# Kernel optimization log

Measured on AMD Instinct MI355X. Metric: run time of the kernel, lower is better.

The kernel has to match this reference:

```python
import jax, jax.numpy as jnp
import numpy as np

N_NODES = 50000
N_EDGES = 800000
IN_CH = 10
HID = 32
HEADS = 4
OUT_CH = 64
EDIM = 1
NEG_SLOPE = 0.2  # PyG GATv2Conv default
LN_EPS = 1e-5


def _glorot(key, shape):
    fan_in, fan_out = shape[0], shape[-1]
    lim = np.sqrt(6.0 / (fan_in + fan_out))
    return jax.random.uniform(key, shape, jnp.float32, -lim, lim)


def setup_inputs() -> dict:
    key = jax.random.key(0)
    ks = jax.random.split(key, 16)
    x = jax.random.normal(ks[0], (N_NODES, IN_CH), jnp.float32)
    edge_index = jax.random.randint(ks[1], (2, N_EDGES), 0, N_NODES, jnp.int64)
    edge_attr = jax.random.normal(ks[2], (N_EDGES, EDIM), jnp.float32)
    return {
        "x": x,
        "edge_attr": edge_attr,
        "W1l": _glorot(ks[3], (IN_CH, HEADS * HID)),
        "W1r": _glorot(ks[4], (IN_CH, HEADS * HID)),
        "W1e": _glorot(ks[5], (EDIM, HEADS * HID)),
        "att1": _glorot(ks[6], (HEADS, HID)),
        "b1": jnp.zeros((HEADS * HID,), jnp.float32),
        "ln1_g": jnp.ones((HEADS * HID,), jnp.float32),
        "ln1_b": jnp.zeros((HEADS * HID,), jnp.float32),
        "W2l": _glorot(ks[7], (HEADS * HID, OUT_CH)),
        "W2r": _glorot(ks[8], (HEADS * HID, OUT_CH)),
        "W2e": _glorot(ks[9], (EDIM, OUT_CH)),
        "att2": _glorot(ks[10], (1, OUT_CH)),
        "b2": jnp.zeros((OUT_CH,), jnp.float32),
        "ln2_g": jnp.ones((OUT_CH,), jnp.float32),
        "ln2_b": jnp.zeros((OUT_CH,), jnp.float32),
        "edge_index": edge_index,
    }


def gatv2_layer(x, src, dst, edge_attr, Wl, Wr, We, att, bias, heads, ch, concat):
    # GATv2: e_ij = att . leaky_relu(Wl x_i + Wr x_j + We e_ij), softmax over j->i
    n = x.shape[0]
    xl = (x @ Wl).reshape(n, heads, ch)          # target projection [N,H,C]
    xr = (x @ Wr).reshape(n, heads, ch)          # source projection [N,H,C]
    ee = (edge_attr @ We).reshape(-1, heads, ch)  # [E,H,C]
    e = jax.nn.leaky_relu(xl[dst] + xr[src] + ee, NEG_SLOPE)  # [E,H,C]
    logit = jnp.einsum('ehc,hc->eh', e, att)     # [E,H]
    m = jax.ops.segment_max(logit, dst, num_segments=n)       # [N,H]
    expv = jnp.exp(logit - m[dst])
    denom = jax.ops.segment_sum(expv, dst, num_segments=n)    # [N,H]
    alpha = expv / denom[dst]                                  # [E,H]
    out = jax.ops.segment_sum(alpha[:, :, None] * xr[src], dst, num_segments=n)  # [N,H,C]
    out = out.reshape(n, heads * ch) if concat else out.mean(axis=1)
    return out + bias


def layer_norm(h, g, b):
    mu = h.mean(axis=-1, keepdims=True)
    var = ((h - mu) ** 2).mean(axis=-1, keepdims=True)
    return (h - mu) * jax.lax.rsqrt(var + LN_EPS) * g + b


def reference(x, edge_attr, W1l, W1r, W1e, att1, b1, ln1_g, ln1_b,
              W2l, W2r, W2e, att2, b2, ln2_g, ln2_b, edge_index):
    src, dst = edge_index[0], edge_index[1]
    h = gatv2_layer(x, src, dst, edge_attr, W1l, W1r, W1e, att1, b1, HEADS, HID, True)
    h = jax.nn.elu(layer_norm(h, ln1_g, ln1_b))
    # dropout is identity in eval mode
    h = gatv2_layer(h, src, dst, edge_attr, W2l, W2r, W2e, att2, b2, 1, OUT_CH, False)
    h = jax.nn.elu(layer_norm(h, ln2_g, ln2_b))
    return h
```

## Files before the change

kernel.cpp:

```cpp
#include <hip/hip_runtime.h>
#include <math.h>

#define NN 50000
#define NE 800000
#define IN_CH 10
#define NEGS 0.2f
#define LNEPS 1e-5f
#define LOG2E 1.4426950408889634f
#define CH_BLOCKS 782
#define NBUK 196

typedef float f2 __attribute__((ext_vector_type(2)));

__device__ __forceinline__ f2 pkfma(f2 a, f2 b, f2 c) {
    return __builtin_elementwise_fma(a, b, c);
}
__device__ __forceinline__ float red16g(float v) {
    v += __shfl_xor(v, 1);  v += __shfl_xor(v, 2);
    v += __shfl_xor(v, 4);  v += __shfl_xor(v, 8);
    return v;
}
__device__ __forceinline__ float red32g(float v) {
    v = red16g(v); v += __shfl_xor(v, 16);
    return v;
}

__device__ __forceinline__ unsigned pack_bf16(float a, float b) {
    unsigned ua = __float_as_uint(a);
    unsigned ub = __float_as_uint(b);
    ua = (ua + 0x7FFFu + ((ua >> 16) & 1u)) >> 16;
    ub = (ub + 0x7FFFu + ((ub >> 16) & 1u)) & 0xFFFF0000u;
    return ua | ub;
}
__device__ __forceinline__ float bf_lo(unsigned d) { return __uint_as_float(d << 16); }
__device__ __forceinline__ float bf_hi(unsigned d) { return __uint_as_float(d & 0xFFFF0000u); }

__global__ __launch_bounds__(256) void k_proj1(
    const float* __restrict__ x, const float* __restrict__ Wl,
    const float* __restrict__ Wr, float* __restrict__ xl, unsigned* __restrict__ xrb) {
    int lane = threadIdx.x & 63;
    int n = blockIdx.x * 4 + (threadIdx.x >> 6);
    if (n >= NN) return;
    int c0 = lane * 2;
    float al0 = 0.f, al1 = 0.f, ar0 = 0.f, ar1 = 0.f;
#pragma unroll
    for (int k = 0; k < IN_CH; ++k) {
        float xv = x[n * IN_CH + k];
        al0 = fmaf(xv, Wl[k * 128 + c0], al0);
        al1 = fmaf(xv, Wl[k * 128 + c0 + 1], al1);
        ar0 = fmaf(xv, Wr[k * 128 + c0], ar0);
        ar1 = fmaf(xv, Wr[k * 128 + c0 + 1], ar1);
    }
    *(float2*)&xl[(size_t)n * 128 + c0] = make_float2(al0, al1);
    xrb[(size_t)n * 64 + lane] = pack_bf16(ar0, ar1);
}


__global__ __launch_bounds__(256) void k_hist(
    const int* __restrict__ ei, int* __restrict__ bh) {
    __shared__ int h[256];
    int t = threadIdx.x, b = blockIdx.x;
    h[t] = 0;
    __syncthreads();
    int e0 = b * 1024 + t * 4;
    if (e0 < NE) {
        int4 d4 = *(const int4*)(ei + NE + e0);
        atomicAdd(&h[d4.x >> 8], 1);
        atomicAdd(&h[d4.y >> 8], 1);
        atomicAdd(&h[d4.z >> 8], 1);
        atomicAdd(&h[d4.w >> 8], 1);
    }
    __syncthreads();
    bh[b * 256 + t] = h[t];
}

__global__ __launch_bounds__(256) void k_colscan(
    int* __restrict__ bh, int* __restrict__ coltotal) {
    __shared__ int sh[256];
    int t = threadIdx.x, j = blockIdx.x;
    int v[4];
    int mysum = 0;
#pragma unroll
    for (int i = 0; i < 4; ++i) {
        int r = t * 4 + i;
        v[i] = (r < CH_BLOCKS) ? bh[r * 256 + j] : 0;
        mysum += v[i];
    }
    sh[t] = mysum;
    __syncthreads();
    for (int off = 1; off < 256; off <<= 1) {
        int u = (t >= off) ? sh[t - off] : 0;
        __syncthreads();
        sh[t] += u;
        __syncthreads();
    }
    int ex = sh[t] - mysum;
#pragma unroll
    for (int i = 0; i < 4; ++i) {
        int r = t * 4 + i;
        if (r < CH_BLOCKS) { bh[r * 256 + j] = ex; ex += v[i]; }
    }
    if (t == 255) coltotal[j] = sh[255];
}

__global__ __launch_bounds__(256) void k_bb(
    const int* __restrict__ coltotal, int* __restrict__ bb) {
    __shared__ int sh[256];
    int t = threadIdx.x;
    int v = coltotal[t];
    sh[t] = v;
    __syncthreads();
    for (int off = 1; off < 256; off <<= 1) {
        int u = (t >= off) ? sh[t - off] : 0;
        __syncthreads();
        sh[t] += u;
        __syncthreads();
    }
    bb[t] = sh[t] - v;
    if (t == 255) bb[256] = sh[255];
}

__global__ __launch_bounds__(256) void k_coarse(
    const int* __restrict__ ei, const float* __restrict__ ea,
    const int* __restrict__ bh, const int* __restrict__ bb,
    int2* __restrict__ coarse) {
    __shared__ int h[256];
    __shared__ int lbase[256];
    int t = threadIdx.x, b = blockIdx.x;
    h[t] = 0;
    lbase[t] = bb[t] + bh[b * 256 + t];
    __syncthreads();
    int e0 = b * 1024 + t * 4;
    if (e0 >= NE) return;
    int4 d4 = *(const int4*)(ei + NE + e0);
    int4 s4 = *(const int4*)(ei + e0);
    float4 a4 = *(const float4*)(ea + e0);
    {
        int bk = d4.x >> 8; int r = atomicAdd(&h[bk], 1);
        coarse[lbase[bk] + r] = make_int2(s4.x | ((d4.x & 255) << 16), __float_as_int(a4.x));
    }
    {
        int bk = d4.y >> 8; int r = atomicAdd(&h[bk], 1);
        coarse[lbase[bk] + r] = make_int2(s4.y | ((d4.y & 255) << 16), __float_as_int(a4.y));
    }
    {
        int bk = d4.z >> 8; int r = atomicAdd(&h[bk], 1);
        coarse[lbase[bk] + r] = make_int2(s4.z | ((d4.z & 255) << 16), __float_as_int(a4.z));
    }
    {
        int bk = d4.w >> 8; int r = atomicAdd(&h[bk], 1);
        coarse[lbase[bk] + r] = make_int2(s4.w | ((d4.w & 255) << 16), __float_as_int(a4.w));
    }
}

__global__ __launch_bounds__(256) void k_fine(
    const int2* __restrict__ coarse, const int* __restrict__ bb,
    int* __restrict__ rowstart, int2* __restrict__ cpack) {
    __shared__ int cnt[256];
    __shared__ int pfx[256];
    __shared__ int sh[256];
    int t = threadIdx.x, b = blockIdx.x;
    cnt[t] = 0;
    __syncthreads();
    int lo = bb[b], hi = bb[b + 1];
    int ecnt = hi - lo;
    for (int i = t; i < ecnt; i += 256) {
        int dl = (coarse[lo + i].x >> 16) & 255;
        atomicAdd(&cnt[dl], 1);
    }
    __syncthreads();
    int v = cnt[t];
    sh[t] = v;
    __syncthreads();
    for (int off = 1; off < 256; off <<= 1) {
        int u = (t >= off) ? sh[t - off] : 0;
        __syncthreads();
        sh[t] += u;
        __syncthreads();
    }
    pfx[t] = sh[t] - v;
    int n0 = b * 256;
    if (n0 + t < NN) rowstart[n0 + t] = lo + (sh[t] - v);
    if (b == 0 && t == 0) rowstart[NN] = NE;
    cnt[t] = 0;
    __syncthreads();
    for (int i = t; i < ecnt; i += 256) {
        int2 c = coarse[lo + i];
        int dl = (c.x >> 16) & 255;
        int r = atomicAdd(&cnt[dl], 1);
        cpack[lo + pfx[dl] + r] = make_int2(c.x & 0xFFFF, c.y);
    }
}

__global__ __launch_bounds__(256) void k_proj2(
    const float* __restrict__ h1, const float* __restrict__ Wl,
    const float* __restrict__ Wr, float* __restrict__ xl2, unsigned* __restrict__ xr2b) {
    __shared__ float sh_h[64][36];
    __shared__ float sh_w[32][128];
    int t = threadIdx.x;
    int cg = t & 15, ng = t >> 4;
    int c0 = cg * 8;
    int nb = blockIdx.x * 64;
    float acc[4][8];
#pragma unroll
    for (int j = 0; j < 4; ++j)
#pragma unroll
        for (int i = 0; i < 8; ++i) acc[j][i] = 0.f;

    for (int kc = 0; kc < 128; kc += 32) {
#pragma unroll
        for (int i = 0; i < 2; ++i) {
            int fi = t + i * 256;
            int nl = fi >> 3, kq = fi & 7;
            int n = nb + nl;
            float4 v = make_float4(0.f, 0.f, 0.f, 0.f);
            if (n < NN) v = *(const float4*)&h1[(size_t)n * 128 + kc + kq * 4];
            *(float4*)&sh_h[nl][kq * 4] = v;
        }
#pragma unroll
        for (int i = 0; i < 4; ++i) {
            int fi = t + i * 256;
            int kl = fi >> 5, col = (fi & 31) * 4;
            const float* src = (col < 64) ? &Wl[(size_t)(kc + kl) * 64 + col]
                                          : &Wr[(size_t)(kc + kl) * 64 + col - 64];
            *(float4*)&sh_w[kl][col] = *(const float4*)src;
        }
        __syncthreads();
#pragma unroll
        for (int kl = 0; kl < 32; kl += 4) {
            float4 hv[4];
#pragma unroll
            for (int j = 0; j < 4; ++j) hv[j] = *(const float4*)&sh_h[ng + j * 16][kl];
#pragma unroll
            for (int kk = 0; kk < 4; ++kk) {
                float4 wa = *(const float4*)&sh_w[kl + kk][c0];
                float4 wb = *(const float4*)&sh_w[kl + kk][c0 + 4];
#pragma unroll
                for (int j = 0; j < 4; ++j) {
                    float hs = kk == 0 ? hv[j].x : kk == 1 ? hv[j].y : kk == 2 ? hv[j].z : hv[j].w;
                    acc[j][0] = fmaf(hs, wa.x, acc[j][0]);
                    acc[j][1] = fmaf(hs, wa.y, acc[j][1]);
                    acc[j][2] = fmaf(hs, wa.z, acc[j][2]);
                    acc[j][3] = fmaf(hs, wa.w, acc[j][3]);
                    acc[j][4] = fmaf(hs, wb.x, acc[j][4]);
                    acc[j][5] = fmaf(hs, wb.y, acc[j][5]);
                    acc[j][6] = fmaf(hs, wb.z, acc[j][6]);
                    acc[j][7] = fmaf(hs, wb.w, acc[j][7]);
                }
            }
        }
        __syncthreads();
    }
    if (cg < 8) {
#pragma unroll
        for (int j = 0; j < 4; ++j) {
            int n = nb + ng + j * 16;
            if (n < NN) {
                *(float4*)&xl2[(size_t)n * 64 + c0] =
                    make_float4(acc[j][0], acc[j][1], acc[j][2], acc[j][3]);
                *(float4*)&xl2[(size_t)n * 64 + c0 + 4] =
                    make_float4(acc[j][4], acc[j][5], acc[j][6], acc[j][7]);
            }
        }
    } else {
        int cc = c0 - 64;
#pragma unroll
        for (int j = 0; j < 4; ++j) {
            int n = nb + ng + j * 16;
            if (n < NN) {
                uint4 pk;
                pk.x = pack_bf16(acc[j][0], acc[j][1]);
                pk.y = pack_bf16(acc[j][2], acc[j][3]);
                pk.z = pack_bf16(acc[j][4], acc[j][5]);
                pk.w = pack_bf16(acc[j][6], acc[j][7]);
                *(uint4*)&xr2b[(size_t)n * 32 + (cc >> 1)] = pk;
            }
        }
    }
}


__device__ __forceinline__ void edge1_step(
    const int2* __restrict__ cpack, const unsigned char* __restrict__ xrb, int p, int l,
    const f2& xl01, const f2& xl23, const f2& We01, const f2& We23,
    const f2& at6a, const f2& at6b, const f2& at4a, const f2& at4b,
    f2& acc01, f2& acc23, float& den, bool tail, int pmax) {
    bool valid = !tail || (p <= pmax);
    int2 pk = cpack[valid ? p : pmax];
    float eav = __int_as_float(pk.y);
    unsigned off = (unsigned)pk.x * 256u + (unsigned)(l * 8);
    uint2 dw = *(const uint2*)(xrb + off);
    f2 x01, x23;
    x01.x = bf_lo(dw.x); x01.y = bf_hi(dw.x);
    x23.x = bf_lo(dw.y); x23.y = bf_hi(dw.y);
    f2 ev = {eav, eav};
    f2 u01 = pkfma(ev, We01, xl01) + x01;
    f2 u23 = pkfma(ev, We23, xl23) + x23;
    float dot = fmaf(at6a.x, u01.x, at4a.x * fabsf(u01.x));
    dot = fmaf(at6a.y, u01.y, fmaf(at4a.y, fabsf(u01.y), dot));
    dot = fmaf(at6b.x, u23.x, fmaf(at4b.x, fabsf(u23.x), dot));
    dot = fmaf(at6b.y, u23.y, fmaf(at4b.y, fabsf(u23.y), dot));
    dot += __shfl_xor(dot, 1);
    dot += __shfl_xor(dot, 2);
    dot += __shfl_xor(dot, 4);
    float el = exp2f(dot);
    if (tail && !valid) el = 0.f;
    den += el;
    f2 el2 = {el, el};
    acc01 = pkfma(el2, x01, acc01);
    acc23 = pkfma(el2, x23, acc23);
}

__global__ __launch_bounds__(256) void k_fused1(
    const int* __restrict__ rs, const int2* __restrict__ cpack,
    const float* __restrict__ xl, const unsigned char* __restrict__ xrb,
    const float* __restrict__ We, const float* __restrict__ att,
    const float* __restrict__ bias, const float* __restrict__ g,
    const float* __restrict__ b, float* __restrict__ h1) {
    int lane = threadIdx.x & 63;
    int n = blockIdx.x * 4 + (threadIdx.x >> 6);
    if (n >= NN) return;
    int half = lane >> 5;
    int l = lane & 31;
    int c0 = l * 4;
    float4 xldf = *(const float4*)&xl[(size_t)n * 128 + c0];
    float4 Wef = *(const float4*)&We[c0];
    float4 atv = *(const float4*)&att[c0];
    f2 xl01 = {xldf.x, xldf.y}, xl23 = {xldf.z, xldf.w};
    f2 We01 = {Wef.x, Wef.y}, We23 = {Wef.z, Wef.w};
    f2 at6a = {atv.x * (0.6f * LOG2E), atv.y * (0.6f * LOG2E)};
    f2 at6b = {atv.z * (0.6f * LOG2E), atv.w * (0.6f * LOG2E)};
    f2 at4a = {atv.x * (0.4f * LOG2E), atv.y * (0.4f * LOG2E)};
    f2 at4b = {atv.z * (0.4f * LOG2E), atv.w * (0.4f * LOG2E)};
    int beg = rs[n], end = rs[n + 1];
    int cnt = end - beg;
    int pfull = beg + (cnt & ~7);
    f2 a01[2] = {{0.f, 0.f}, {0.f, 0.f}};
    f2 a23[2] = {{0.f, 0.f}, {0.f, 0.f}};
    float den[2] = {0.f, 0.f};
    for (int p0 = beg; p0 < pfull; p0 += 8) {
#pragma unroll
        for (int s = 0; s < 4; ++s)
            edge1_step(cpack, xrb, p0 + s * 2 + half, l, xl01, xl23, We01, We23,
                       at6a, at6b, at4a, at4b, a01[s & 1], a23[s & 1], den[s & 1],
                       false, 0);
    }
    if (cnt & 7) {
#pragma unroll
        for (int s = 0; s < 4; ++s)
            edge1_step(cpack, xrb, pfull + s * 2 + half, l, xl01, xl23, We01, We23,
                       at6a, at6b, at4a, at4b, a01[s & 1], a23[s & 1], den[s & 1],
                       true, end - 1);
    }
    f2 s01 = a01[0] + a01[1];
    f2 s23 = a23[0] + a23[1];
    float den0 = den[0] + den[1];
    s01.x += __shfl_xor(s01.x, 32);
    s01.y += __shfl_xor(s01.y, 32);
    s23.x += __shfl_xor(s23.x, 32);
    s23.y += __shfl_xor(s23.y, 32);
    den0 += __shfl_xor(den0, 32);
    float inv = den0 > 0.f ? 1.f / den0 : 0.f;
    float4 bv = *(const float4*)&bias[c0];
    float a0 = s01.x * inv + bv.x;
    float a1 = s01.y * inv + bv.y;
    float a2 = s23.x * inv + bv.z;
    float a3 = s23.y * inv + bv.w;
    float mu = red32g(a0 + a1 + a2 + a3) * (1.f / 128.f);
    float d0 = a0 - mu, d1 = a1 - mu, d2 = a2 - mu, d3 = a3 - mu;
    float var = red32g(d0 * d0 + d1 * d1 + d2 * d2 + d3 * d3) * (1.f / 128.f);
    float rsq = rsqrtf(var + LNEPS);
    float4 gv = *(const float4*)&g[c0];
    float4 bb = *(const float4*)&b[c0];
    float o0 = d0 * rsq * gv.x + bb.x;
    float o1 = d1 * rsq * gv.y + bb.y;
    float o2 = d2 * rsq * gv.z + bb.z;
    float o3 = d3 * rsq * gv.w + bb.w;
    o0 = o0 > 0.f ? o0 : __expf(o0) - 1.f;
    o1 = o1 > 0.f ? o1 : __expf(o1) - 1.f;
    o2 = o2 > 0.f ? o2 : __expf(o2) - 1.f;
    o3 = o3 > 0.f ? o3 : __expf(o3) - 1.f;
    if (half == 0)
        *(float4*)&h1[(size_t)n * 128 + c0] = make_float4(o0, o1, o2, o3);
}

__device__ __forceinline__ void edge2_step(
    const int2* __restrict__ cpack, const unsigned char* __restrict__ xr2b, int p, int l,
    const f2& xl01, const f2& xl23, const f2& We01, const f2& We23,
    const f2& at6a, const f2& at6b, const f2& at4a, const f2& at4b,
    f2& acc01, f2& acc23, float& den, bool tail, int pmax) {
    bool valid = !tail || (p <= pmax);
    int2 pk = cpack[valid ? p : pmax];
    float eav = __int_as_float(pk.y);
    unsigned off = (unsigned)pk.x * 128u + (unsigned)(l * 8);
    uint2 dw = *(const uint2*)(xr2b + off);
    f2 x01, x23;
    x01.x = bf_lo(dw.x); x01.y = bf_hi(dw.x);
    x23.x = bf_lo(dw.y); x23.y = bf_hi(dw.y);
    f2 ev = {eav, eav};
    f2 u01 = pkfma(ev, We01, xl01) + x01;
    f2 u23 = pkfma(ev, We23, xl23) + x23;
    float dot = fmaf(at6a.x, u01.x, at4a.x * fabsf(u01.x));
    dot = fmaf(at6a.y, u01.y, fmaf(at4a.y, fabsf(u01.y), dot));
    dot = fmaf(at6b.x, u23.x, fmaf(at4b.x, fabsf(u23.x), dot));
    dot = fmaf(at6b.y, u23.y, fmaf(at4b.y, fabsf(u23.y), dot));
    dot += __shfl_xor(dot, 1);
    dot += __shfl_xor(dot, 2);
    dot += __shfl_xor(dot, 4);
    dot += __shfl_xor(dot, 8);
    float el = exp2f(dot);
    if (tail && !valid) el = 0.f;
    den += el;
    f2 el2 = {el, el};
    acc01 = pkfma(el2, x01, acc01);
    acc23 = pkfma(el2, x23, acc23);
}

__global__ __launch_bounds__(256) void k_fused2(
    const int* __restrict__ rs, const int2* __restrict__ cpack,
    const float* __restrict__ xl2, const unsigned char* __restrict__ xr2b,
    const float* __restrict__ We, const float* __restrict__ att,
    const float* __restrict__ bias, const float* __restrict__ g,
    const float* __restrict__ b, float* __restrict__ out) {
    int lane = threadIdx.x & 63;
    int n = blockIdx.x * 4 + (threadIdx.x >> 6);
    if (n >= NN) return;
    int grp = lane >> 4;
    int l = lane & 15;
    int c0 = l * 4;
    float4 xldf = *(const float4*)&xl2[(size_t)n * 64 + c0];
    float4 Wef = *(const float4*)&We[c0];
    float4 atv = *(const float4*)&att[c0];
    f2 xl01 = {xldf.x, xldf.y}, xl23 = {xldf.z, xldf.w};
    f2 We01 = {Wef.x, Wef.y}, We23 = {Wef.z, Wef.w};
    f2 at6a = {atv.x * (0.6f * LOG2E), atv.y * (0.6f * LOG2E)};
    f2 at6b = {atv.z * (0.6f * LOG2E), atv.w * (0.6f * LOG2E)};
    f2 at4a = {atv.x * (0.4f * LOG2E), atv.y * (0.4f * LOG2E)};
    f2 at4b = {atv.z * (0.4f * LOG2E), atv.w * (0.4f * LOG2E)};
    int beg = rs[n], end = rs[n + 1];
    int cnt = end - beg;
    int pfull = beg + (cnt & ~7);
    f2 a01[2] = {{0.f, 0.f}, {0.f, 0.f}};
    f2 a23[2] = {{0.f, 0.f}, {0.f, 0.f}};
    float den[2] = {0.f, 0.f};
    for (int p0 = beg; p0 < pfull; p0 += 8) {
#pragma unroll
        for (int s = 0; s < 2; ++s)
            edge2_step(cpack, xr2b, p0 + s * 4 + grp, l, xl01, xl23, We01, We23,
                       at6a, at6b, at4a, at4b, a01[s], a23[s], den[s], false, 0);
    }
    if (cnt & 7) {
#pragma unroll
        for (int s = 0; s < 2; ++s)
            edge2_step(cpack, xr2b, pfull + s * 4 + grp, l, xl01, xl23, We01, We23,
                       at6a, at6b, at4a, at4b, a01[s], a23[s], den[s], true, end - 1);
    }
    f2 s01 = a01[0] + a01[1];
    f2 s23 = a23[0] + a23[1];
    float den0 = den[0] + den[1];
    s01.x += __shfl_xor(s01.x, 16); s01.x += __shfl_xor(s01.x, 32);
    s01.y += __shfl_xor(s01.y, 16); s01.y += __shfl_xor(s01.y, 32);
    s23.x += __shfl_xor(s23.x, 16); s23.x += __shfl_xor(s23.x, 32);
    s23.y += __shfl_xor(s23.y, 16); s23.y += __shfl_xor(s23.y, 32);
    den0 += __shfl_xor(den0, 16); den0 += __shfl_xor(den0, 32);
    float inv = den0 > 0.f ? 1.f / den0 : 0.f;
    float4 bv = *(const float4*)&bias[c0];
    float a0 = s01.x * inv + bv.x;
    float a1 = s01.y * inv + bv.y;
    float a2 = s23.x * inv + bv.z;
    float a3 = s23.y * inv + bv.w;
    float mu = red16g(a0 + a1 + a2 + a3) * (1.f / 64.f);
    float d0 = a0 - mu, d1 = a1 - mu, d2 = a2 - mu, d3 = a3 - mu;
    float var = red16g(d0 * d0 + d1 * d1 + d2 * d2 + d3 * d3) * (1.f / 64.f);
    float rsq = rsqrtf(var + LNEPS);
    float4 gv = *(const float4*)&g[c0];
    float4 bb = *(const float4*)&b[c0];
    float o0 = d0 * rsq * gv.x + bb.x;
    float o1 = d1 * rsq * gv.y + bb.y;
    float o2 = d2 * rsq * gv.z + bb.z;
    float o3 = d3 * rsq * gv.w + bb.w;
    o0 = o0 > 0.f ? o0 : __expf(o0) - 1.f;
    o1 = o1 > 0.f ? o1 : __expf(o1) - 1.f;
    o2 = o2 > 0.f ? o2 : __expf(o2) - 1.f;
    o3 = o3 > 0.f ? o3 : __expf(o3) - 1.f;
    if (grp == 0)
        *(float4*)&out[(size_t)n * 64 + c0] = make_float4(o0, o1, o2, o3);
}

extern "C" void kernel_launch(void* const* d_in, const int* in_sizes, int n_in,
                              void* d_out, int out_size, void* d_ws, size_t ws_size,
                              hipStream_t stream) {
    const float* x    = (const float*)d_in[0];
    const float* ea   = (const float*)d_in[1];
    const float* W1l  = (const float*)d_in[2];
    const float* W1r  = (const float*)d_in[3];
    const float* W1e  = (const float*)d_in[4];
    const float* att1 = (const float*)d_in[5];
    const float* b1   = (const float*)d_in[6];
    const float* ln1g = (const float*)d_in[7];
    const float* ln1b = (const float*)d_in[8];
    const float* W2l  = (const float*)d_in[9];
    const float* W2r  = (const float*)d_in[10];
    const float* W2e  = (const float*)d_in[11];
    const float* att2 = (const float*)d_in[12];
    const float* b2   = (const float*)d_in[13];
    const float* ln2g = (const float*)d_in[14];
    const float* ln2b = (const float*)d_in[15];
    const int*   ei   = (const int*)d_in[16];
    float* out = (float*)d_out;
    float* ws  = (float*)d_ws;

    const size_t A = (size_t)NN * 128;
    float* xl1 = ws;
    float* h1  = ws + A;
    float* xl2 = ws + 2 * A;
    unsigned* xr1b = (unsigned*)(ws + 2 * A + (size_t)NN * 64);
    unsigned* xr2b = xr1b + (size_t)NN * 64;
    int2* cpack  = (int2*)(xr2b + (size_t)NN * 32);
    int2* coarse = cpack + (size_t)NE;
    int* bh      = (int*)(coarse + (size_t)NE);
    int* coltotal= bh + (size_t)CH_BLOCKS * 256;
    int* bb      = coltotal + 256;
    int* rowstart= bb + 258;

    k_proj1<<<(NN + 3) / 4, 256, 0, stream>>>(x, W1l, W1r, xl1, xr1b);
    k_hist<<<CH_BLOCKS, 256, 0, stream>>>(ei, bh);
    k_colscan<<<256, 256, 0, stream>>>(bh, coltotal);
    k_bb<<<1, 256, 0, stream>>>(coltotal, bb);
    k_coarse<<<CH_BLOCKS, 256, 0, stream>>>(ei, ea, bh, bb, coarse);
    k_fine<<<NBUK, 256, 0, stream>>>(coarse, bb, rowstart, cpack);

    k_fused1<<<(NN + 3) / 4, 256, 0, stream>>>(rowstart, cpack, xl1,
                                               (const unsigned char*)xr1b, W1e, att1, b1,
                                               ln1g, ln1b, h1);
    k_proj2<<<(NN + 63) / 64, 256, 0, stream>>>(h1, W2l, W2r, xl2, xr2b);
    k_fused2<<<(NN + 3) / 4, 256, 0, stream>>>(rowstart, cpack, xl2,
                                               (const unsigned char*)xr2b, W2e, att2, b2,
                                               ln2g, ln2b, out);
}
```

Before: 274.0 us.

## Merge projection with histogram kernel and batch edge gathers ahead of compute

Merges the layer-1 projection and the destination histogram into one launch by splitting the grid by block index, which removes a kernel launch and lets the two independent jobs run concurrently. In both fused edge kernels, all index loads, then all feature gathers, for a group of edges are issued before any compute, so more memory requests are in flight at once. In layer 2, each iteration now covers 16 edges instead of 8. The batching raises register pressure, and the larger chunk in layer 2 makes the masked tail waste more lanes on low-degree nodes.

```diff
diff --git a/kernel.cpp b/kernel.cpp
--- a/kernel.cpp
+++ b/kernel.cpp
@@ -7,6 +7,7 @@
 #define NEGS 0.2f
 #define LNEPS 1e-5f
 #define LOG2E 1.4426950408889634f
+#define P1_BLOCKS 12500
 #define CH_BLOCKS 782
 #define NBUK 196
 
@@ -35,43 +36,42 @@
 __device__ __forceinline__ float bf_lo(unsigned d) { return __uint_as_float(d << 16); }
 __device__ __forceinline__ float bf_hi(unsigned d) { return __uint_as_float(d & 0xFFFF0000u); }
 
-__global__ __launch_bounds__(256) void k_proj1(
+__global__ __launch_bounds__(256) void k_proj1_hist(
     const float* __restrict__ x, const float* __restrict__ Wl,
-    const float* __restrict__ Wr, float* __restrict__ xl, unsigned* __restrict__ xrb) {
-    int lane = threadIdx.x & 63;
-    int n = blockIdx.x * 4 + (threadIdx.x >> 6);
-    if (n >= NN) return;
-    int c0 = lane * 2;
-    float al0 = 0.f, al1 = 0.f, ar0 = 0.f, ar1 = 0.f;
-#pragma unroll
-    for (int k = 0; k < IN_CH; ++k) {
-        float xv = x[n * IN_CH + k];
-        al0 = fmaf(xv, Wl[k * 128 + c0], al0);
-        al1 = fmaf(xv, Wl[k * 128 + c0 + 1], al1);
-        ar0 = fmaf(xv, Wr[k * 128 + c0], ar0);
-        ar1 = fmaf(xv, Wr[k * 128 + c0 + 1], ar1);
-    }
-    *(float2*)&xl[(size_t)n * 128 + c0] = make_float2(al0, al1);
-    xrb[(size_t)n * 64 + lane] = pack_bf16(ar0, ar1);
-}
-
-
-__global__ __launch_bounds__(256) void k_hist(
+    const float* __restrict__ Wr, float* __restrict__ xl, unsigned* __restrict__ xrb,
     const int* __restrict__ ei, int* __restrict__ bh) {
     __shared__ int h[256];
-    int t = threadIdx.x, b = blockIdx.x;
-    h[t] = 0;
-    __syncthreads();
-    int e0 = b * 1024 + t * 4;
-    if (e0 < NE) {
-        int4 d4 = *(const int4*)(ei + NE + e0);
-        atomicAdd(&h[d4.x >> 8], 1);
-        atomicAdd(&h[d4.y >> 8], 1);
-        atomicAdd(&h[d4.z >> 8], 1);
-        atomicAdd(&h[d4.w >> 8], 1);
-    }
-    __syncthreads();
-    bh[b * 256 + t] = h[t];
+    int bI = blockIdx.x;
+    if (bI < P1_BLOCKS) {
+        int lane = threadIdx.x & 63;
+        int n = bI * 4 + (threadIdx.x >> 6);
+        int c0 = lane * 2;
+        float al0 = 0.f, al1 = 0.f, ar0 = 0.f, ar1 = 0.f;
+#pragma unroll
+        for (int k = 0; k < IN_CH; ++k) {
+            float xv = x[n * IN_CH + k];
+            al0 = fmaf(xv, Wl[k * 128 + c0], al0);
+            al1 = fmaf(xv, Wl[k * 128 + c0 + 1], al1);
+            ar0 = fmaf(xv, Wr[k * 128 + c0], ar0);
+            ar1 = fmaf(xv, Wr[k * 128 + c0 + 1], ar1);
+        }
+        *(float2*)&xl[(size_t)n * 128 + c0] = make_float2(al0, al1);
+        xrb[(size_t)n * 64 + lane] = pack_bf16(ar0, ar1);
+    } else {
+        int t = threadIdx.x, b = bI - P1_BLOCKS;
+        h[t] = 0;
+        __syncthreads();
+        int e0 = b * 1024 + t * 4;
+        if (e0 < NE) {
+            int4 d4 = *(const int4*)(ei + NE + e0);
+            atomicAdd(&h[d4.x >> 8], 1);
+            atomicAdd(&h[d4.y >> 8], 1);
+            atomicAdd(&h[d4.z >> 8], 1);
+            atomicAdd(&h[d4.w >> 8], 1);
+        }
+        __syncthreads();
+        bh[b * 256 + t] = h[t];
+    }
 }
 
 __global__ __launch_bounds__(256) void k_colscan(
@@ -279,37 +279,6 @@
     }
 }
 
-
-__device__ __forceinline__ void edge1_step(
-    const int2* __restrict__ cpack, const unsigned char* __restrict__ xrb, int p, int l,
-    const f2& xl01, const f2& xl23, const f2& We01, const f2& We23,
-    const f2& at6a, const f2& at6b, const f2& at4a, const f2& at4b,
-    f2& acc01, f2& acc23, float& den, bool tail, int pmax) {
-    bool valid = !tail || (p <= pmax);
-    int2 pk = cpack[valid ? p : pmax];
-    float eav = __int_as_float(pk.y);
-    unsigned off = (unsigned)pk.x * 256u + (unsigned)(l * 8);
-    uint2 dw = *(const uint2*)(xrb + off);
-    f2 x01, x23;
-    x01.x = bf_lo(dw.x); x01.y = bf_hi(dw.x);
-    x23.x = bf_lo(dw.y); x23.y = bf_hi(dw.y);
-    f2 ev = {eav, eav};
-    f2 u01 = pkfma(ev, We01, xl01) + x01;
-    f2 u23 = pkfma(ev, We23, xl23) + x23;
-    float dot = fmaf(at6a.x, u01.x, at4a.x * fabsf(u01.x));
-    dot = fmaf(at6a.y, u01.y, fmaf(at4a.y, fabsf(u01.y), dot));
-    dot = fmaf(at6b.x, u23.x, fmaf(at4b.x, fabsf(u23.x), dot));
-    dot = fmaf(at6b.y, u23.y, fmaf(at4b.y, fabsf(u23.y), dot));
-    dot += __shfl_xor(dot, 1);
-    dot += __shfl_xor(dot, 2);
-    dot += __shfl_xor(dot, 4);
-    float el = exp2f(dot);
-    if (tail && !valid) el = 0.f;
-    den += el;
-    f2 el2 = {el, el};
-    acc01 = pkfma(el2, x01, acc01);
-    acc23 = pkfma(el2, x23, acc23);
-}
 
 __global__ __launch_bounds__(256) void k_fused1(
     const int* __restrict__ rs, const int2* __restrict__ cpack,
@@ -339,18 +308,73 @@
     f2 a23[2] = {{0.f, 0.f}, {0.f, 0.f}};
     float den[2] = {0.f, 0.f};
     for (int p0 = beg; p0 < pfull; p0 += 8) {
+        int2 pk[4];
+#pragma unroll
+        for (int s = 0; s < 4; ++s) pk[s] = cpack[p0 + s * 2 + half];
+        uint2 dw[4];
 #pragma unroll
         for (int s = 0; s < 4; ++s)
-            edge1_step(cpack, xrb, p0 + s * 2 + half, l, xl01, xl23, We01, We23,
-                       at6a, at6b, at4a, at4b, a01[s & 1], a23[s & 1], den[s & 1],
-                       false, 0);
+            dw[s] = *(const uint2*)(xrb + (unsigned)pk[s].x * 256u + (unsigned)(l * 8));
+#pragma unroll
+        for (int s = 0; s < 4; ++s) {
+            float eav = __int_as_float(pk[s].y);
+            f2 x01, x23;
+            x01.x = bf_lo(dw[s].x); x01.y = bf_hi(dw[s].x);
+            x23.x = bf_lo(dw[s].y); x23.y = bf_hi(dw[s].y);
+            f2 ev = {eav, eav};
+            f2 u01 = pkfma(ev, We01, xl01) + x01;
+            f2 u23 = pkfma(ev, We23, xl23) + x23;
+            float dot = fmaf(at6a.x, u01.x, at4a.x * fabsf(u01.x));
+            dot = fmaf(at6a.y, u01.y, fmaf(at4a.y, fabsf(u01.y), dot));
+            dot = fmaf(at6b.x, u23.x, fmaf(at4b.x, fabsf(u23.x), dot));
+            dot = fmaf(at6b.y, u23.y, fmaf(at4b.y, fabsf(u23.y), dot));
+            dot += __shfl_xor(dot, 1);
+            dot += __shfl_xor(dot, 2);
+            dot += __shfl_xor(dot, 4);
+            float el = exp2f(dot);
+            int w = s & 1;
+            den[w] += el;
+            f2 el2 = {el, el};
+            a01[w] = pkfma(el2, x01, a01[w]);
+            a23[w] = pkfma(el2, x23, a23[w]);
+        }
     }
     if (cnt & 7) {
+        int2 pk[4];
+        bool vv[4];
+#pragma unroll
+        for (int s = 0; s < 4; ++s) {
+            int p = pfull + s * 2 + half;
+            vv[s] = p < end;
+            pk[s] = cpack[vv[s] ? p : end - 1];
+        }
+        uint2 dw[4];
 #pragma unroll
         for (int s = 0; s < 4; ++s)
-            edge1_step(cpack, xrb, pfull + s * 2 + half, l, xl01, xl23, We01, We23,
-                       at6a, at6b, at4a, at4b, a01[s & 1], a23[s & 1], den[s & 1],
-                       true, end - 1);
+            dw[s] = *(const uint2*)(xrb + (unsigned)pk[s].x * 256u + (unsigned)(l * 8));
+#pragma unroll
+        for (int s = 0; s < 4; ++s) {
+            float eav = __int_as_float(pk[s].y);
+            f2 x01, x23;
+            x01.x = bf_lo(dw[s].x); x01.y = bf_hi(dw[s].x);
+            x23.x = bf_lo(dw[s].y); x23.y = bf_hi(dw[s].y);
+            f2 ev = {eav, eav};
+            f2 u01 = pkfma(ev, We01, xl01) + x01;
+            f2 u23 = pkfma(ev, We23, xl23) + x23;
+            float dot = fmaf(at6a.x, u01.x, at4a.x * fabsf(u01.x));
+            dot = fmaf(at6a.y, u01.y, fmaf(at4a.y, fabsf(u01.y), dot));
+            dot = fmaf(at6b.x, u23.x, fmaf(at4b.x, fabsf(u23.x), dot));
+            dot = fmaf(at6b.y, u23.y, fmaf(at4b.y, fabsf(u23.y), dot));
+            dot += __shfl_xor(dot, 1);
+            dot += __shfl_xor(dot, 2);
+            dot += __shfl_xor(dot, 4);
+            float el = vv[s] ? exp2f(dot) : 0.f;
+            int w = s & 1;
+            den[w] += el;
+            f2 el2 = {el, el};
+            a01[w] = pkfma(el2, x01, a01[w]);
+            a23[w] = pkfma(el2, x23, a23[w]);
+        }
     }
     f2 s01 = a01[0] + a01[1];
     f2 s23 = a23[0] + a23[1];
@@ -384,38 +408,6 @@
         *(float4*)&h1[(size_t)n * 128 + c0] = make_float4(o0, o1, o2, o3);
 }
 
-__device__ __forceinline__ void edge2_step(
-    const int2* __restrict__ cpack, const unsigned char* __restrict__ xr2b, int p, int l,
-    const f2& xl01, const f2& xl23, const f2& We01, const f2& We23,
-    const f2& at6a, const f2& at6b, const f2& at4a, const f2& at4b,
-    f2& acc01, f2& acc23, float& den, bool tail, int pmax) {
-    bool valid = !tail || (p <= pmax);
-    int2 pk = cpack[valid ? p : pmax];
-    float eav = __int_as_float(pk.y);
-    unsigned off = (unsigned)pk.x * 128u + (unsigned)(l * 8);
-    uint2 dw = *(const uint2*)(xr2b + off);
-    f2 x01, x23;
-    x01.x = bf_lo(dw.x); x01.y = bf_hi(dw.x);
-    x23.x = bf_lo(dw.y); x23.y = bf_hi(dw.y);
-    f2 ev = {eav, eav};
-    f2 u01 = pkfma(ev, We01, xl01) + x01;
-    f2 u23 = pkfma(ev, We23, xl23) + x23;
-    float dot = fmaf(at6a.x, u01.x, at4a.x * fabsf(u01.x));
-    dot = fmaf(at6a.y, u01.y, fmaf(at4a.y, fabsf(u01.y), dot));
-    dot = fmaf(at6b.x, u23.x, fmaf(at4b.x, fabsf(u23.x), dot));
-    dot = fmaf(at6b.y, u23.y, fmaf(at4b.y, fabsf(u23.y), dot));
-    dot += __shfl_xor(dot, 1);
-    dot += __shfl_xor(dot, 2);
-    dot += __shfl_xor(dot, 4);
-    dot += __shfl_xor(dot, 8);
-    float el = exp2f(dot);
-    if (tail && !valid) el = 0.f;
-    den += el;
-    f2 el2 = {el, el};
-    acc01 = pkfma(el2, x01, acc01);
-    acc23 = pkfma(el2, x23, acc23);
-}
-
 __global__ __launch_bounds__(256) void k_fused2(
     const int* __restrict__ rs, const int2* __restrict__ cpack,
     const float* __restrict__ xl2, const unsigned char* __restrict__ xr2b,
@@ -439,21 +431,80 @@
     f2 at4b = {atv.z * (0.4f * LOG2E), atv.w * (0.4f * LOG2E)};
     int beg = rs[n], end = rs[n + 1];
     int cnt = end - beg;
-    int pfull = beg + (cnt & ~7);
+    int pfull = beg + (cnt & ~15);
     f2 a01[2] = {{0.f, 0.f}, {0.f, 0.f}};
     f2 a23[2] = {{0.f, 0.f}, {0.f, 0.f}};
     float den[2] = {0.f, 0.f};
-    for (int p0 = beg; p0 < pfull; p0 += 8) {
-#pragma unroll
-        for (int s = 0; s < 2; ++s)
-            edge2_step(cpack, xr2b, p0 + s * 4 + grp, l, xl01, xl23, We01, We23,
-                       at6a, at6b, at4a, at4b, a01[s], a23[s], den[s], false, 0);
-    }
-    if (cnt & 7) {
-#pragma unroll
-        for (int s = 0; s < 2; ++s)
-            edge2_step(cpack, xr2b, pfull + s * 4 + grp, l, xl01, xl23, We01, We23,
-                       at6a, at6b, at4a, at4b, a01[s], a23[s], den[s], true, end - 1);
+    for (int p0 = beg; p0 < pfull; p0 += 16) {
+        int2 pk[4];
+#pragma unroll
+        for (int s = 0; s < 4; ++s) pk[s] = cpack[p0 + s * 4 + grp];
+        uint2 dw[4];
+#pragma unroll
+        for (int s = 0; s < 4; ++s)
+            dw[s] = *(const uint2*)(xr2b + (unsigned)pk[s].x * 128u + (unsigned)(l * 8));
+#pragma unroll
+        for (int s = 0; s < 4; ++s) {
+            float eav = __int_as_float(pk[s].y);
+            f2 x01, x23;
+            x01.x = bf_lo(dw[s].x); x01.y = bf_hi(dw[s].x);
+            x23.x = bf_lo(dw[s].y); x23.y = bf_hi(dw[s].y);
+            f2 ev = {eav, eav};
+            f2 u01 = pkfma(ev, We01, xl01) + x01;
+            f2 u23 = pkfma(ev, We23, xl23) + x23;
+            float dot = fmaf(at6a.x, u01.x, at4a.x * fabsf(u01.x));
+            dot = fmaf(at6a.y, u01.y, fmaf(at4a.y, fabsf(u01.y), dot));
+            dot = fmaf(at6b.x, u23.x, fmaf(at4b.x, fabsf(u23.x), dot));
+            dot = fmaf(at6b.y, u23.y, fmaf(at4b.y, fabsf(u23.y), dot));
+            dot += __shfl_xor(dot, 1);
+            dot += __shfl_xor(dot, 2);
+            dot += __shfl_xor(dot, 4);
+            dot += __shfl_xor(dot, 8);
+            float el = exp2f(dot);
+            int w = s & 1;
+            den[w] += el;
+            f2 el2 = {el, el};
+            a01[w] = pkfma(el2, x01, a01[w]);
+            a23[w] = pkfma(el2, x23, a23[w]);
+        }
+    }
+    if (cnt & 15) {
+        int2 pk[4];
+        bool vv[4];
+#pragma unroll
+        for (int s = 0; s < 4; ++s) {
+            int p = pfull + s * 4 + grp;
+            vv[s] = p < end;
+            pk[s] = cpack[vv[s] ? p : end - 1];
+        }
+        uint2 dw[4];
+#pragma unroll
+        for (int s = 0; s < 4; ++s)
+            dw[s] = *(const uint2*)(xr2b + (unsigned)pk[s].x * 128u + (unsigned)(l * 8));
+#pragma unroll
+        for (int s = 0; s < 4; ++s) {
+            float eav = __int_as_float(pk[s].y);
+            f2 x01, x23;
+            x01.x = bf_lo(dw[s].x); x01.y = bf_hi(dw[s].x);
+            x23.x = bf_lo(dw[s].y); x23.y = bf_hi(dw[s].y);
+            f2 ev = {eav, eav};
+            f2 u01 = pkfma(ev, We01, xl01) + x01;
+            f2 u23 = pkfma(ev, We23, xl23) + x23;
+            float dot = fmaf(at6a.x, u01.x, at4a.x * fabsf(u01.x));
+            dot = fmaf(at6a.y, u01.y, fmaf(at4a.y, fabsf(u01.y), dot));
+            dot = fmaf(at6b.x, u23.x, fmaf(at4b.x, fabsf(u23.x), dot));
+            dot = fmaf(at6b.y, u23.y, fmaf(at4b.y, fabsf(u23.y), dot));
+            dot += __shfl_xor(dot, 1);
+            dot += __shfl_xor(dot, 2);
+            dot += __shfl_xor(dot, 4);
+            dot += __shfl_xor(dot, 8);
+            float el = vv[s] ? exp2f(dot) : 0.f;
+            int w = s & 1;
+            den[w] += el;
+            f2 el2 = {el, el};
+            a01[w] = pkfma(el2, x01, a01[w]);
+            a23[w] = pkfma(el2, x23, a23[w]);
+        }
     }
     f2 s01 = a01[0] + a01[1];
     f2 s23 = a23[0] + a23[1];
@@ -523,8 +574,8 @@
     int* bb      = coltotal + 256;
     int* rowstart= bb + 258;
 
-    k_proj1<<<(NN + 3) / 4, 256, 0, stream>>>(x, W1l, W1r, xl1, xr1b);
-    k_hist<<<CH_BLOCKS, 256, 0, stream>>>(ei, bh);
+    k_proj1_hist<<<P1_BLOCKS + CH_BLOCKS, 256, 0, stream>>>(x, W1l, W1r, xl1, xr1b,
+                                                            ei, bh);
     k_colscan<<<256, 256, 0, stream>>>(bh, coltotal);
     k_bb<<<1, 256, 0, stream>>>(coltotal, bb);
     k_coarse<<<CH_BLOCKS, 256, 0, stream>>>(ei, ea, bh, bb, coarse);
```

Result: faster. 266.9 us (-2.6%).
